# Kernel optimization log

Measured on AMD Instinct MI355X. Metric: run time of the kernel, lower is better.

## Reference

```python
import jax, jax.numpy as jnp
import numpy as np

N = 50000
IN_DIM = 256
HID = 64
HEADS = 4
OUT_DIM = 64
NEG_SLOPE = 0.2


def gat_conv(x, src, dst, W, att_src, att_dst, bias, heads, out_ch):
    # x: [N, F_in]; src/dst: [E] (self-loops already appended)
    n = x.shape[0]
    h = (x @ W).reshape(n, heads, out_ch)                     # [N,H,C]
    a_s = jnp.sum(h * att_src, axis=-1)                       # [N,H]
    a_d = jnp.sum(h * att_dst, axis=-1)                       # [N,H]
    e = jax.nn.leaky_relu(a_s[src] + a_d[dst], NEG_SLOPE)     # [E,H]
    # segment softmax over destination neighborhoods
    m = jax.ops.segment_max(e, dst, num_segments=n)           # [N,H]
    m = jnp.where(jnp.isfinite(m), m, 0.0)
    ex = jnp.exp(e - m[dst])                                  # [E,H]
    denom = jax.ops.segment_sum(ex, dst, num_segments=n)      # [N,H]
    alpha = ex / (denom[dst] + 1e-16)                         # [E,H]
    msg = alpha[:, :, None] * h[src]                          # [E,H,C]
    out = jax.ops.segment_sum(msg, dst, num_segments=n)       # [N,H,C]
    return out.reshape(n, heads * out_ch) + bias


def setup_inputs() -> dict:
    key = jax.random.key(0)
    ks = jax.random.split(key, 10)
    glorot = lambda k, shape: jax.random.normal(k, shape, jnp.float32) * np.sqrt(2.0 / (shape[0] + shape[-1]))
    x = jax.random.normal(ks[0], (N, IN_DIM), jnp.float32)
    edge_index = jax.random.randint(ks[1], (2, 800000), 0, N, jnp.int64)
    W1 = glorot(ks[2], (IN_DIM, HEADS * HID))
    att_src1 = glorot(ks[3], (HEADS, HID))
    att_dst1 = glorot(ks[4], (HEADS, HID))
    b1 = jnp.zeros((HEADS * HID,), jnp.float32)
    W2 = glorot(ks[5], (HEADS * HID, OUT_DIM))
    att_src2 = glorot(ks[6], (1, OUT_DIM))
    att_dst2 = glorot(ks[7], (1, OUT_DIM))
    b2 = jnp.zeros((OUT_DIM,), jnp.float32)
    return {"x": x, "edge_index": edge_index, "W1": W1, "att_src1": att_src1,
            "att_dst1": att_dst1, "b1": b1, "W2": W2, "att_src2": att_src2,
            "att_dst2": att_dst2, "b2": b2}


def reference(x, edge_index, W1, att_src1, att_dst1, b1, W2, att_src2, att_dst2, b2):
    # add self loops (PyG GATConv default)
    loops = jnp.arange(N, dtype=edge_index.dtype)
    src = jnp.concatenate([edge_index[0], loops])
    dst = jnp.concatenate([edge_index[1], loops])
    h = gat_conv(x, src, dst, W1, att_src1, att_dst1, b1, HEADS, HID)
    h = jax.nn.elu(h)
    out = gat_conv(h, src, dst, W2, att_src2, att_dst2, b2, 1, OUT_DIM)
    return out
```

## Files before the change

kernel.cpp:

```cpp
#include <hip/hip_runtime.h>
#include <math.h>

#define N_NODES 50000
#define E_RAW   800000
#define E_TOT   850000
#define NEG_SLOPE 0.2f
#define NBC 196
#define GEMM1_BLKS 3125
#define SCAT_BLKS  3321

typedef __attribute__((ext_vector_type(8))) short short8;
typedef __attribute__((ext_vector_type(4))) float f32x4;

__device__ __forceinline__ float lrelu(float v) {
    return v >= 0.f ? v : NEG_SLOPE * v;
}
__device__ __forceinline__ unsigned short f2bf(float f) {
    union { float f; unsigned u; } v; v.f = f;
    unsigned r = v.u + 0x7FFF + ((v.u >> 16) & 1);
    return (unsigned short)(r >> 16);
}
__device__ __forceinline__ float bf2f(unsigned short h) {
    union { unsigned u; float f; } v; v.u = ((unsigned)h) << 16;
    return v.f;
}
__device__ __forceinline__ int C1(int p) { return (p & 15) * 16 + (p >> 4); }
__device__ __forceinline__ int C2(int p) { return (p & 3) * 16 + (p >> 2); }

__global__ __launch_bounds__(256) void k_prep_hist(
    const int* __restrict__ dst, int* __restrict__ counts,
    const float* __restrict__ W1, const float* __restrict__ W2,
    unsigned short* __restrict__ Wf1, unsigned short* __restrict__ Wf2)
{
    int idx = blockIdx.x * 256 + threadIdx.x;
    if (idx < 8192) {
        int lane = idx & 63, kb = (idx >> 6) & 7, nb = idx >> 9;
        int c = nb * 16 + (lane & 15);
        int k0 = kb * 32 + ((lane >> 4) & 3) * 8;
        short8 pk;
#pragma unroll
        for (int j = 0; j < 8; ++j)
            pk[j] = (short)f2bf(W1[(k0 + j) * 256 + c]);
        *(short8*)&Wf1[idx * 8] = pk;
    } else if (idx < 10240) {
        int i2 = idx - 8192;
        int lane = i2 & 63, kb = (i2 >> 6) & 7, nb = i2 >> 9;
        int c = nb * 16 + (lane & 15);
        int k0 = kb * 32 + ((lane >> 4) & 3) * 8;
        short8 pk;
#pragma unroll
        for (int j = 0; j < 8; ++j)
            pk[j] = (short)f2bf(W2[C1(k0 + j) * 64 + c]);
        *(short8*)&Wf2[i2 * 8] = pk;
    }
    if (idx < E_TOT) {
        int d = (idx < E_RAW) ? dst[idx] : idx - E_RAW;
        atomicAdd(&counts[d], 1);
    }
}

__global__ __launch_bounds__(256) void k_scan1(
    const int* __restrict__ counts, int* __restrict__ off, int* __restrict__ bsum)
{
    __shared__ int sh[256];
    int t = threadIdx.x, i = blockIdx.x * 256 + t;
    int c = (i < N_NODES) ? counts[i] : 0;
    sh[t] = c; __syncthreads();
    for (int ofs = 1; ofs < 256; ofs <<= 1) {
        int v = (t >= ofs) ? sh[t - ofs] : 0;
        __syncthreads(); sh[t] += v; __syncthreads();
    }
    if (i < N_NODES) off[i] = sh[t] - c;
    if (t == 255) bsum[blockIdx.x] = sh[255];
}

__global__ __launch_bounds__(256) void k_scan23(
    int* __restrict__ off, const int* __restrict__ bsum)
{
    __shared__ int sh[256];
    int t = threadIdx.x, b = blockIdx.x;
    sh[t] = (t < b) ? bsum[t] : 0;
    __syncthreads();
    for (int ofs = 128; ofs > 0; ofs >>= 1) {
        if (t < ofs) sh[t] += sh[t + ofs];
        __syncthreads();
    }
    int base = sh[0];
    int i = b * 256 + t;
    if (i < N_NODES) off[i] += base;
    if (b == 0 && t == 0) off[N_NODES] = E_TOT;
}

__global__ __launch_bounds__(256) void k_gemm1_scatter(
    const float* __restrict__ x, const unsigned short* __restrict__ Wf1,
    const float* __restrict__ att_src, const float* __restrict__ att_dst,
    unsigned short* __restrict__ h1b, float* __restrict__ as1, float* __restrict__ ad1,
    const int* __restrict__ src, const int* __restrict__ dst,
    const int* __restrict__ off, int* __restrict__ counts,
    unsigned short* __restrict__ esrc)
{
    if (blockIdx.x >= GEMM1_BLKS) {
        int e = (blockIdx.x - GEMM1_BLKS) * 256 + threadIdx.x;
        if (e < E_TOT) {
            int s, d;
            if (e < E_RAW) { s = src[e]; d = dst[e]; } else { s = e - E_RAW; d = s; }
            int old = atomicSub(&counts[d], 1);
            esrc[off[d] + old - 1] = (unsigned short)s;
        }
        return;
    }
    const int t = threadIdx.x;
    const int lane = t & 63;
    const int w = t >> 6;
    const int rbase = blockIdx.x * 16;
    const int q  = lane & 15;
    const int kg = lane >> 4;
    const int rowA = rbase + q;

    f32x4 acc[4];
#pragma unroll
    for (int nb = 0; nb < 4; ++nb) acc[nb] = (f32x4){0.f, 0.f, 0.f, 0.f};

    short8 b[2][4];
    float4 a0, a1, a0n, a1n;
    {
        const float* ap = &x[rowA * 256 + kg * 8];
        a0 = *(const float4*)ap;
        a1 = *(const float4*)(ap + 4);
#pragma unroll
        for (int nb = 0; nb < 4; ++nb)
            b[0][nb] = *(const short8*)&Wf1[(((w * 4 + nb) * 8 + 0) * 64 + lane) * 8];
    }
#pragma unroll
    for (int kb = 0; kb < 8; ++kb) {
        if (kb < 7) {
            const float* ap = &x[rowA * 256 + (kb + 1) * 32 + kg * 8];
            a0n = *(const float4*)ap;
            a1n = *(const float4*)(ap + 4);
#pragma unroll
            for (int nb = 0; nb < 4; ++nb)
                b[(kb + 1) & 1][nb] =
                    *(const short8*)&Wf1[(((w * 4 + nb) * 8 + kb + 1) * 64 + lane) * 8];
        }
        short8 af;
        af[0] = (short)f2bf(a0.x); af[1] = (short)f2bf(a0.y);
        af[2] = (short)f2bf(a0.z); af[3] = (short)f2bf(a0.w);
        af[4] = (short)f2bf(a1.x); af[5] = (short)f2bf(a1.y);
        af[6] = (short)f2bf(a1.z); af[7] = (short)f2bf(a1.w);
#pragma unroll
        for (int nb = 0; nb < 4; ++nb)
            acc[nb] = __builtin_amdgcn_mfma_f32_16x16x32_bf16(af, b[kb & 1][nb], acc[nb], 0, 0, 0);
        if (kb < 7) { a0 = a0n; a1 = a1n; }
    }

#pragma unroll
    for (int reg = 0; reg < 4; ++reg) {
        int n = rbase + kg * 4 + reg;
        ushort4 pk;
        pk.x = f2bf(acc[0][reg]); pk.y = f2bf(acc[1][reg]);
        pk.z = f2bf(acc[2][reg]); pk.w = f2bf(acc[3][reg]);
        *(ushort4*)&h1b[n * 256 + q * 16 + w * 4] = pk;
    }
    float asv[4], adv[4];
#pragma unroll
    for (int nb = 0; nb < 4; ++nb) {
        int col = (w * 4 + nb) * 16 + q;
        asv[nb] = att_src[col];
        adv[nb] = att_dst[col];
    }
#pragma unroll
    for (int reg = 0; reg < 4; ++reg) {
        float s = acc[0][reg]*asv[0] + acc[1][reg]*asv[1] + acc[2][reg]*asv[2] + acc[3][reg]*asv[3];
        float d = acc[0][reg]*adv[0] + acc[1][reg]*adv[1] + acc[2][reg]*adv[2] + acc[3][reg]*adv[3];
#pragma unroll
        for (int ofs = 1; ofs < 16; ofs <<= 1) {
            s += __shfl_xor(s, ofs);
            d += __shfl_xor(d, ofs);
        }
        if (q == 0) {
            int n = rbase + kg * 4 + reg;
            as1[n * 4 + w] = s;
            ad1[n * 4 + w] = d;
        }
    }
}

__global__ __launch_bounds__(256) void k_gat1g2(
    const unsigned short* __restrict__ esrc, const int* __restrict__ off,
    const float* __restrict__ as1, const float* __restrict__ ad1,
    const unsigned short* __restrict__ h1b, const float* __restrict__ b1,
    const unsigned short* __restrict__ Wf2,
    const float* __restrict__ att_src2, const float* __restrict__ att_dst2,
    unsigned short* __restrict__ h2b, float* __restrict__ as2, float* __restrict__ ad2)
{
    __shared__ unsigned short hs[16][264];
    __shared__ float ss[16][4], sd[16][4];
    const int t = threadIdx.x;
    const int w = t >> 6;
    const int lane = t & 63;
    const int d0 = blockIdx.x * 16;
    const int head = lane & 3;

    for (int r = 0; r < 4; ++r) {
        const int ld = w * 4 + r;
        const int d = d0 + ld;
        const float adv = ad1[d * 4 + head];
        const int e0 = off[d], e1 = off[d + 1];
        float4 acc = make_float4(0.f, 0.f, 0.f, 0.f);
        float dn = 0.f;
        int e = e0;
        for (; e + 3 < e1; e += 4) {
            int s0 = esrc[e], s1 = esrc[e + 1], s2 = esrc[e + 2], s3 = esrc[e + 3];
            float w0 = __expf(lrelu(as1[s0 * 4 + head] + adv));
            float w1 = __expf(lrelu(as1[s1 * 4 + head] + adv));
            float w2 = __expf(lrelu(as1[s2 * 4 + head] + adv));
            float w3 = __expf(lrelu(as1[s3 * 4 + head] + adv));
            ushort4 u0 = *(const ushort4*)&h1b[s0 * 256 + lane * 4];
            ushort4 u1 = *(const ushort4*)&h1b[s1 * 256 + lane * 4];
            ushort4 u2 = *(const ushort4*)&h1b[s2 * 256 + lane * 4];
            ushort4 u3 = *(const ushort4*)&h1b[s3 * 256 + lane * 4];
            dn += (w0 + w1) + (w2 + w3);
            acc.x = fmaf(w0, bf2f(u0.x), fmaf(w1, bf2f(u1.x), fmaf(w2, bf2f(u2.x), fmaf(w3, bf2f(u3.x), acc.x))));
            acc.y = fmaf(w0, bf2f(u0.y), fmaf(w1, bf2f(u1.y), fmaf(w2, bf2f(u2.y), fmaf(w3, bf2f(u3.y), acc.y))));
            acc.z = fmaf(w0, bf2f(u0.z), fmaf(w1, bf2f(u1.z), fmaf(w2, bf2f(u2.z), fmaf(w3, bf2f(u3.z), acc.z))));
            acc.w = fmaf(w0, bf2f(u0.w), fmaf(w1, bf2f(u1.w), fmaf(w2, bf2f(u2.w), fmaf(w3, bf2f(u3.w), acc.w))));
        }
        for (; e < e1; ++e) {
            int s0 = esrc[e];
            float w0 = __expf(lrelu(as1[s0 * 4 + head] + adv));
            ushort4 u0 = *(const ushort4*)&h1b[s0 * 256 + lane * 4];
            dn += w0;
            acc.x = fmaf(w0, bf2f(u0.x), acc.x);
            acc.y = fmaf(w0, bf2f(u0.y), acc.y);
            acc.z = fmaf(w0, bf2f(u0.z), acc.z);
            acc.w = fmaf(w0, bf2f(u0.w), acc.w);
        }
        const float inv = 1.f / (dn + 1e-16f);
        float o[4] = {acc.x, acc.y, acc.z, acc.w};
        ushort4 pk;
        unsigned short* pko = (unsigned short*)&pk;
#pragma unroll
        for (int i = 0; i < 4; ++i) {
            float v = o[i] * inv + b1[C1(lane * 4 + i)];
            v = v > 0.f ? v : expm1f(v);
            pko[i] = f2bf(v);
        }
        *(ushort4*)&hs[ld][lane * 4] = pk;
    }
    __syncthreads();

    const int q  = lane & 15;
    const int kg = lane >> 4;
    f32x4 acc2 = (f32x4){0.f, 0.f, 0.f, 0.f};
#pragma unroll
    for (int kb = 0; kb < 8; ++kb) {
        short8 af = *(const short8*)&hs[q][kb * 32 + kg * 8];
        short8 bf = *(const short8*)&Wf2[((w * 8 + kb) * 64 + lane) * 8];
        acc2 = __builtin_amdgcn_mfma_f32_16x16x32_bf16(af, bf, acc2, 0, 0, 0);
    }
    const float asv = att_src2[w * 16 + q];
    const float adv = att_dst2[w * 16 + q];
#pragma unroll
    for (int reg = 0; reg < 4; ++reg) {
        int row = kg * 4 + reg;
        int n = d0 + row;
        h2b[n * 64 + q * 4 + w] = f2bf(acc2[reg]);
        float s = acc2[reg] * asv;
        float d = acc2[reg] * adv;
#pragma unroll
        for (int ofs = 1; ofs < 16; ofs <<= 1) {
            s += __shfl_xor(s, ofs);
            d += __shfl_xor(d, ofs);
        }
        if (q == 0) { ss[row][w] = s; sd[row][w] = d; }
    }
    __syncthreads();
    if (t < 16) {
        as2[d0 + t] = (ss[t][0] + ss[t][1]) + (ss[t][2] + ss[t][3]);
        ad2[d0 + t] = (sd[t][0] + sd[t][1]) + (sd[t][2] + sd[t][3]);
    }
}

__global__ __launch_bounds__(256) void k_gather2(
    const unsigned short* __restrict__ esrc, const int* __restrict__ off,
    const float* __restrict__ as2, const float* __restrict__ ad2,
    const unsigned short* __restrict__ h2b, const float* __restrict__ b2,
    float* __restrict__ out)
{
    const int t = threadIdx.x;
    const int w = t >> 6;
    const int lane = t & 63;
    const int g  = lane >> 4;
    const int j2 = lane & 15;
    const int d = blockIdx.x * 16 + w * 4 + g;
    const float adv = ad2[d];
    const int e0 = off[d], e1 = off[d + 1];
    const unsigned short* hb = h2b + j2 * 4;

    float acc[4] = {0.f, 0.f, 0.f, 0.f};
    float dn = 0.f;
    int e = e0;
    for (; e + 3 < e1; e += 4) {
        int s0 = esrc[e], s1 = esrc[e + 1], s2 = esrc[e + 2], s3 = esrc[e + 3];
        float w0 = __expf(lrelu(as2[s0] + adv));
        float w1 = __expf(lrelu(as2[s1] + adv));
        float w2 = __expf(lrelu(as2[s2] + adv));
        float w3 = __expf(lrelu(as2[s3] + adv));
        ushort4 u0 = *(const ushort4*)(hb + s0 * 64);
        ushort4 u1 = *(const ushort4*)(hb + s1 * 64);
        ushort4 u2 = *(const ushort4*)(hb + s2 * 64);
        ushort4 u3 = *(const ushort4*)(hb + s3 * 64);
        dn += (w0 + w1) + (w2 + w3);
        acc[0] = fmaf(w0, bf2f(u0.x), fmaf(w1, bf2f(u1.x), fmaf(w2, bf2f(u2.x), fmaf(w3, bf2f(u3.x), acc[0]))));
        acc[1] = fmaf(w0, bf2f(u0.y), fmaf(w1, bf2f(u1.y), fmaf(w2, bf2f(u2.y), fmaf(w3, bf2f(u3.y), acc[1]))));
        acc[2] = fmaf(w0, bf2f(u0.z), fmaf(w1, bf2f(u1.z), fmaf(w2, bf2f(u2.z), fmaf(w3, bf2f(u3.z), acc[2]))));
        acc[3] = fmaf(w0, bf2f(u0.w), fmaf(w1, bf2f(u1.w), fmaf(w2, bf2f(u2.w), fmaf(w3, bf2f(u3.w), acc[3]))));
    }
    for (; e < e1; ++e) {
        int s0 = esrc[e];
        float w0 = __expf(lrelu(as2[s0] + adv));
        ushort4 u0 = *(const ushort4*)(hb + s0 * 64);
        dn += w0;
        acc[0] = fmaf(w0, bf2f(u0.x), acc[0]);
        acc[1] = fmaf(w0, bf2f(u0.y), acc[1]);
        acc[2] = fmaf(w0, bf2f(u0.z), acc[2]);
        acc[3] = fmaf(w0, bf2f(u0.w), acc[3]);
    }
    const float inv = 1.f / (dn + 1e-16f);
#pragma unroll
    for (int i = 0; i < 4; ++i) {
        int col = i * 16 + j2;
        out[d * 64 + col] = acc[i] * inv + b2[col];
    }
}

extern "C" void kernel_launch(void* const* d_in, const int* in_sizes, int n_in,
                              void* d_out, int out_size, void* d_ws, size_t ws_size,
                              hipStream_t stream)
{
    const float* x        = (const float*)d_in[0];
    const int*   ei       = (const int*)d_in[1];
    const float* W1       = (const float*)d_in[2];
    const float* att_src1 = (const float*)d_in[3];
    const float* att_dst1 = (const float*)d_in[4];
    const float* b1       = (const float*)d_in[5];
    const float* W2       = (const float*)d_in[6];
    const float* att_src2 = (const float*)d_in[7];
    const float* att_dst2 = (const float*)d_in[8];
    const float* b2       = (const float*)d_in[9];
    const int* src = ei;
    const int* dst = ei + E_RAW;
    float* out = (float*)d_out;

    char* ws = (char*)d_ws;
    int*            counts = (int*)(ws + 0);
    int*            off    = (int*)(ws + 200000);
    int*            bsum   = (int*)(ws + 400032);
    float*          as1    = (float*)(ws + 400896);
    float*          ad1    = (float*)(ws + 1200896);
    float*          as2    = (float*)(ws + 2000896);
    float*          ad2    = (float*)(ws + 2200896);
    unsigned short* esrc   = (unsigned short*)(ws + 2400896);
    unsigned short* Wf1    = (unsigned short*)(ws + 4100896);
    unsigned short* Wf2    = (unsigned short*)(ws + 4231968);
    unsigned short* h1b    = (unsigned short*)(ws + 4264736);
    unsigned short* h2b    = (unsigned short*)(ws + 29864736);

    hipMemsetAsync(counts, 0, 200000, stream);

    const int EB = (E_TOT + 255) / 256;
    k_prep_hist<<<EB, 256, 0, stream>>>(dst, counts, W1, W2, Wf1, Wf2);
    k_scan1  <<<NBC, 256, 0, stream>>>(counts, off, bsum);
    k_scan23 <<<NBC, 256, 0, stream>>>(off, bsum);
    k_gemm1_scatter<<<GEMM1_BLKS + SCAT_BLKS, 256, 0, stream>>>(
        x, Wf1, att_src1, att_dst1, h1b, as1, ad1,
        src, dst, off, counts, esrc);
    k_gat1g2 <<<3125, 256, 0, stream>>>(esrc, off, as1, ad1, h1b, b1, Wf2,
                                        att_src2, att_dst2, h2b, as2, ad2);
    k_gather2<<<3125, 256, 0, stream>>>(esrc, off, as2, ad2, h2b, b2, out);
}
```

Measured before the change: 234.2 us.

## Tile GEMM1 over 64 rows per block with LDS-staged bf16 input

The first-layer GEMM block now covers 64 node rows instead of 16. It stages x into shared memory as bf16 once, then reuses each loaded W fragment across four row groups of MFMAs. This cuts redundant W loads and per-block overhead four-fold and coalesces the x loads. In exchange it uses about 33KB of LDS and 64 accumulator registers per thread, which can lower occupancy, and it adds bounds clamping for the partial last tile.

```diff
diff --git a/kernel.cpp b/kernel.cpp
--- a/kernel.cpp
+++ b/kernel.cpp
@@ -6,8 +6,8 @@
 #define E_TOT   850000
 #define NEG_SLOPE 0.2f
 #define NBC 196
-#define GEMM1_BLKS 3125
-#define SCAT_BLKS  3321
+#define G1_BLKS 782
+#define SCAT_BLKS 3321
 
 typedef __attribute__((ext_vector_type(8))) short short8;
 typedef __attribute__((ext_vector_type(4))) float f32x4;
@@ -99,8 +99,8 @@
     const int* __restrict__ off, int* __restrict__ counts,
     unsigned short* __restrict__ esrc)
 {
-    if (blockIdx.x >= GEMM1_BLKS) {
-        int e = (blockIdx.x - GEMM1_BLKS) * 256 + threadIdx.x;
+    if (blockIdx.x >= G1_BLKS) {
+        int e = (blockIdx.x - G1_BLKS) * 256 + threadIdx.x;
         if (e < E_TOT) {
             int s, d;
             if (e < E_RAW) { s = src[e]; d = dst[e]; } else { s = e - E_RAW; d = s; }
@@ -109,58 +109,49 @@
         }
         return;
     }
+    __shared__ unsigned short hsx[64 * 264];
     const int t = threadIdx.x;
+    const int rbase = blockIdx.x * 64;
+
+#pragma unroll
+    for (int it = 0; it < 16; ++it) {
+        int idx = it * 1024 + t * 4;
+        int row = idx >> 8, col = idx & 255;
+        int rA = rbase + row;
+        if (rA >= N_NODES) rA = N_NODES - 1;
+        float4 v = *(const float4*)&x[rA * 256 + col];
+        ushort4 pk;
+        pk.x = f2bf(v.x); pk.y = f2bf(v.y); pk.z = f2bf(v.z); pk.w = f2bf(v.w);
+        *(ushort4*)&hsx[row * 264 + col] = pk;
+    }
+    __syncthreads();
+
     const int lane = t & 63;
     const int w = t >> 6;
-    const int rbase = blockIdx.x * 16;
     const int q  = lane & 15;
     const int kg = lane >> 4;
-    const int rowA = rbase + q;
-
-    f32x4 acc[4];
-#pragma unroll
-    for (int nb = 0; nb < 4; ++nb) acc[nb] = (f32x4){0.f, 0.f, 0.f, 0.f};
-
-    short8 b[2][4];
-    float4 a0, a1, a0n, a1n;
-    {
-        const float* ap = &x[rowA * 256 + kg * 8];
-        a0 = *(const float4*)ap;
-        a1 = *(const float4*)(ap + 4);
+
+    f32x4 acc[4][4];
+#pragma unroll
+    for (int rg = 0; rg < 4; ++rg)
+#pragma unroll
+        for (int nb = 0; nb < 4; ++nb) acc[rg][nb] = (f32x4){0.f, 0.f, 0.f, 0.f};
+
+#pragma unroll
+    for (int kb = 0; kb < 8; ++kb) {
+        short8 b[4];
 #pragma unroll
         for (int nb = 0; nb < 4; ++nb)
-            b[0][nb] = *(const short8*)&Wf1[(((w * 4 + nb) * 8 + 0) * 64 + lane) * 8];
-    }
-#pragma unroll
-    for (int kb = 0; kb < 8; ++kb) {
-        if (kb < 7) {
-            const float* ap = &x[rowA * 256 + (kb + 1) * 32 + kg * 8];
-            a0n = *(const float4*)ap;
-            a1n = *(const float4*)(ap + 4);
+            b[nb] = *(const short8*)&Wf1[(((w * 4 + nb) * 8 + kb) * 64 + lane) * 8];
+#pragma unroll
+        for (int rg = 0; rg < 4; ++rg) {
+            short8 af = *(const short8*)&hsx[(rg * 16 + q) * 264 + kb * 32 + kg * 8];
 #pragma unroll
             for (int nb = 0; nb < 4; ++nb)
-                b[(kb + 1) & 1][nb] =
-                    *(const short8*)&Wf1[(((w * 4 + nb) * 8 + kb + 1) * 64 + lane) * 8];
-        }
-        short8 af;
-        af[0] = (short)f2bf(a0.x); af[1] = (short)f2bf(a0.y);
-        af[2] = (short)f2bf(a0.z); af[3] = (short)f2bf(a0.w);
-        af[4] = (short)f2bf(a1.x); af[5] = (short)f2bf(a1.y);
-        af[6] = (short)f2bf(a1.z); af[7] = (short)f2bf(a1.w);
-#pragma unroll
-        for (int nb = 0; nb < 4; ++nb)
-            acc[nb] = __builtin_amdgcn_mfma_f32_16x16x32_bf16(af, b[kb & 1][nb], acc[nb], 0, 0, 0);
-        if (kb < 7) { a0 = a0n; a1 = a1n; }
-    }
-
-#pragma unroll
-    for (int reg = 0; reg < 4; ++reg) {
-        int n = rbase + kg * 4 + reg;
-        ushort4 pk;
-        pk.x = f2bf(acc[0][reg]); pk.y = f2bf(acc[1][reg]);
-        pk.z = f2bf(acc[2][reg]); pk.w = f2bf(acc[3][reg]);
-        *(ushort4*)&h1b[n * 256 + q * 16 + w * 4] = pk;
-    }
+                acc[rg][nb] = __builtin_amdgcn_mfma_f32_16x16x32_bf16(af, b[nb], acc[rg][nb], 0, 0, 0);
+        }
+    }
+
     float asv[4], adv[4];
 #pragma unroll
     for (int nb = 0; nb < 4; ++nb) {
@@ -169,18 +160,30 @@
         adv[nb] = att_dst[col];
     }
 #pragma unroll
-    for (int reg = 0; reg < 4; ++reg) {
-        float s = acc[0][reg]*asv[0] + acc[1][reg]*asv[1] + acc[2][reg]*asv[2] + acc[3][reg]*asv[3];
-        float d = acc[0][reg]*adv[0] + acc[1][reg]*adv[1] + acc[2][reg]*adv[2] + acc[3][reg]*adv[3];
-#pragma unroll
-        for (int ofs = 1; ofs < 16; ofs <<= 1) {
-            s += __shfl_xor(s, ofs);
-            d += __shfl_xor(d, ofs);
-        }
-        if (q == 0) {
-            int n = rbase + kg * 4 + reg;
-            as1[n * 4 + w] = s;
-            ad1[n * 4 + w] = d;
+    for (int rg = 0; rg < 4; ++rg) {
+#pragma unroll
+        for (int reg = 0; reg < 4; ++reg) {
+            int n = rbase + rg * 16 + kg * 4 + reg;
+            bool ok = n < N_NODES;
+            if (ok) {
+                ushort4 pk;
+                pk.x = f2bf(acc[rg][0][reg]); pk.y = f2bf(acc[rg][1][reg]);
+                pk.z = f2bf(acc[rg][2][reg]); pk.w = f2bf(acc[rg][3][reg]);
+                *(ushort4*)&h1b[n * 256 + q * 16 + w * 4] = pk;
+            }
+            float s = acc[rg][0][reg]*asv[0] + acc[rg][1][reg]*asv[1]
+                    + acc[rg][2][reg]*asv[2] + acc[rg][3][reg]*asv[3];
+            float d = acc[rg][0][reg]*adv[0] + acc[rg][1][reg]*adv[1]
+                    + acc[rg][2][reg]*adv[2] + acc[rg][3][reg]*adv[3];
+#pragma unroll
+            for (int ofs = 1; ofs < 16; ofs <<= 1) {
+                s += __shfl_xor(s, ofs);
+                d += __shfl_xor(d, ofs);
+            }
+            if (ok && q == 0) {
+                as1[n * 4 + w] = s;
+                ad1[n * 4 + w] = d;
+            }
         }
     }
 }
@@ -372,7 +375,7 @@
     k_prep_hist<<<EB, 256, 0, stream>>>(dst, counts, W1, W2, Wf1, Wf2);
     k_scan1  <<<NBC, 256, 0, stream>>>(counts, off, bsum);
     k_scan23 <<<NBC, 256, 0, stream>>>(off, bsum);
-    k_gemm1_scatter<<<GEMM1_BLKS + SCAT_BLKS, 256, 0, stream>>>(
+    k_gemm1_scatter<<<G1_BLKS + SCAT_BLKS, 256, 0, stream>>>(
         x, Wf1, att_src1, att_dst1, h1b, as1, ad1,
         src, dst, off, counts, esrc);
     k_gat1g2 <<<3125, 256, 0, stream>>>(esrc, off, as1, ad1, h1b, b1, Wf2,
```

New measurement: 220.3 us, median of 2. 6.0% less time.
